# Optimization experiments

Measured on AMD Instinct MI355X. Metric: run time of the kernel, lower is better.

## Reference

```python
import jax, jax.numpy as jnp
import numpy as np

B, Y = 1024, 50000
MAX_TRIALS = 4096


def setup_inputs() -> dict:
    key = jax.random.key(0)
    k1, k2 = jax.random.split(key)
    input_ = jax.random.normal(k1, (B, Y), dtype=jnp.float32)
    pos = jax.random.randint(k2, (B,), 0, Y)
    target = jnp.zeros((B, Y), jnp.float32).at[jnp.arange(B), pos].set(1.0)
    return {"input_": input_, "target": target, "max_num_trials": MAX_TRIALS}


def reference(input_, target, max_num_trials):
    """WARP loss. The torch original sequentially samples negatives WITHOUT
    replacement per row until margin 1 + s_neg - s_pos >= 0 or max_num_trials
    is hit. Sampling without replacement == taking a uniform random
    permutation of the negative labels and scanning it; the first violating
    position t gives num_trials = t+1. This lets us fully vectorize the
    irregular loop while computing identical math (up to RNG stream)."""
    Bn, Yn = input_.shape
    rows = jnp.arange(Bn)
    pos = jnp.argmax(target, axis=1)                 # one positive per row (as J[i,1])
    pos_score = input_[rows, pos]                    # [B]

    # uniform random permutation of the Y-1 negatives per row:
    # random sort keys, force the positive label to sort last, drop it.
    u = jax.random.uniform(jax.random.key(42), (Bn, Yn))
    u = u.at[rows, pos].set(2.0)
    perm = jnp.argsort(u, axis=1)[:, : Yn - 1]       # [B, Y-1] negative label ids

    neg_scores = jnp.take_along_axis(input_, perm, axis=1)   # [B, Y-1]
    margins = 1.0 + neg_scores - pos_score[:, None]
    trial_ok = jnp.arange(Yn - 1)[None, :] < max_num_trials
    viol = (margins >= 0.0) & trial_ok
    found = jnp.any(viol, axis=1)
    first = jnp.argmax(viol, axis=1)                 # first violating trial index
    num_trials = (first + 1).astype(jnp.float32)
    # loss_weight = log(floor((Y-1)/num_trials)); 0 when no violator found
    L = jnp.where(found, jnp.log(jnp.floor((Yn - 1.0) / num_trials)), 0.0)
    neg_score = jnp.where(
        found, jnp.take_along_axis(neg_scores, first[:, None], axis=1)[:, 0], 0.0
    )
    loss = L * (1.0 - pos_score + neg_score)         # [B]
    return jnp.sum(loss, keepdims=True)              # shape (1,), as torch.sum(dim=0, keepdim=True)
```

## Files before the change

### kernel.cpp

```cpp
#include <hip/hip_runtime.h>
#include <stdint.h>

#define BN 1024
#define YN 50000
#define NTOT (BN * YN)
#define NGROUPS (NTOT / 4)
#define CAP 96
#define BITS_T (1u << 22)
#define HASH_BLOCKS 4096
#define STRIDE (HASH_BLOCKS * 256)

#define ROTL(x, r) __builtin_amdgcn_alignbit((x), (x), 32u - (r))
#define RND(b, a, r) { b += a; a = ROTL(a, r); a ^= b; }
#define RND4(r) { RND(b0,a0,r) RND(b1,a1,r) RND(b2,a2,r) RND(b3,a3,r) }
#define INJ4(db, da) { b0 += (db); b1 += (db); b2 += (db); b3 += (db); \
                       a0 += (da); a1 += (da); a2 += (da); a3 += (da); }

__device__ __forceinline__ uint32_t tf_bits(uint32_t ctr) {
    const uint32_t ks1 = 42u, ks2 = 0x1BD11BF0u;
    uint32_t x0 = 0u, x1 = ctr + ks1;
#define TFR(r) { x0 += x1; x1 = ROTL(x1, r); x1 ^= x0; }
    TFR(13) TFR(15) TFR(26) TFR(6)
    x0 += ks1; x1 += ks2 + 1u;
    TFR(17) TFR(29) TFR(16) TFR(24)
    x0 += ks2; x1 += 2u;
    TFR(13) TFR(15) TFR(26) TFR(6)
    x1 += ks1 + 3u;
    TFR(17) TFR(29) TFR(16) TFR(24)
    x0 += ks1; x1 += ks2 + 4u;
    TFR(13) TFR(15) TFR(26) TFR(6)
    x0 += ks2; x1 += 5u;
    return x0 ^ x1;
}

struct WS {
    uint32_t* cnt; int* pos; float* ps; float* row_loss; int* flag; uint32_t* cand;
};
static inline WS ws_layout(void* d_ws) {
    uint32_t* p = (uint32_t*)d_ws;
    WS w;
    w.cnt = p; w.pos = (int*)(p + BN); w.ps = (float*)(p + 2 * BN);
    w.row_loss = (float*)(p + 3 * BN); w.flag = (int*)(p + 4 * BN);
    w.cand = p + 5 * BN;
    return w;
}

__global__ __launch_bounds__(256, 4) void gen_kernel(
    const float* __restrict__ input, const float* __restrict__ target,
    uint32_t* __restrict__ cnt, uint32_t* __restrict__ cand,
    int* __restrict__ pos_out, float* __restrict__ ps_out)
{
    const int tid = threadIdx.x;
    if (blockIdx.x < BN) {
        const int row = blockIdx.x;
        const size_t base = (size_t)row * YN;
        __shared__ volatile int s_pos;
        if (tid == 0) s_pos = -1;
        __syncthreads();
        const float4* t4 = (const float4*)(target + base);
        for (int j4 = tid; j4 < YN / 4; j4 += 256) {
            if (s_pos >= 0) break;
            float4 v = t4[j4];
            int c0 = 4 * j4;
            if (v.x != 0.0f) s_pos = c0;
            if (v.y != 0.0f) s_pos = c0 + 1;
            if (v.z != 0.0f) s_pos = c0 + 2;
            if (v.w != 0.0f) s_pos = c0 + 3;
        }
        __syncthreads();
        if (tid == 0) {
            int p = s_pos;
            pos_out[row] = p;
            ps_out[row] = input[base + p];
        }
        return;
    }
    const uint32_t gid = (uint32_t)(blockIdx.x - BN) * 256u + (uint32_t)tid;
    const uint32_t ks1 = 42u, ks2 = 0x1BD11BF0u;
    for (uint32_t g = gid; g < NGROUPS; g += STRIDE) {
        const uint32_t c4 = g << 2;
        uint32_t a0 = c4 + 42u, a1 = c4 + 43u, a2 = c4 + 44u, a3 = c4 + 45u;
        uint32_t b0 = 0u, b1 = 0u, b2 = 0u, b3 = 0u;
        RND4(13) RND4(15) RND4(26) RND4(6)
        INJ4(ks1, ks2 + 1u)
        RND4(17) RND4(29) RND4(16) RND4(24)
        INJ4(ks2, 2u)
        RND4(13) RND4(15) RND4(26) RND4(6)
        INJ4(0u, ks1 + 3u)
        RND4(17) RND4(29) RND4(16) RND4(24)
        INJ4(ks1, ks2 + 4u)
        RND4(13) RND4(15) RND4(26) RND4(6)
        INJ4(ks2, 5u)
        const uint32_t o0 = b0 ^ a0, o1 = b1 ^ a1, o2 = b2 ^ a2, o3 = b3 ^ a3;
        const uint32_t m01 = o0 < o1 ? o0 : o1;
        const uint32_t m23 = o2 < o3 ? o2 : o3;
        const uint32_t m = m01 < m23 ? m01 : m23;
        if (__builtin_expect(m < BITS_T, 0)) {
            const uint32_t os[4] = {o0, o1, o2, o3};
#pragma unroll
            for (int k = 0; k < 4; ++k) {
                if (os[k] < BITS_T) {
                    const uint32_t idx = c4 + (uint32_t)k;
                    const uint32_t row = idx / 50000u;
                    const uint32_t col = idx - row * 50000u;
                    const uint32_t slot = atomicAdd(&cnt[row], 1u);
                    if (slot < CAP)
                        cand[row * CAP + slot] = ((os[k] >> 9) << 17) | col;
                }
            }
        }
    }
}

__global__ __launch_bounds__(256) void resolve_kernel(
    const float* __restrict__ input, const uint32_t* __restrict__ cnt,
    const uint32_t* __restrict__ cand, const int* __restrict__ pos_,
    const float* __restrict__ ps_, const int* __restrict__ mt_ptr,
    float* __restrict__ row_loss, int* __restrict__ flag)
{
    const int gtid = blockIdx.x * 256 + threadIdx.x;
    const int row = gtid >> 6;
    const int lane = gtid & 63;
    const uint32_t n = cnt[row];
    if (n > CAP) { if (lane == 0) flag[row] = 1; return; }
    const int pos = pos_[row];
    const float ps = ps_[row];
    const uint32_t* cl = cand + row * CAP;
    const float* rowp = input + (size_t)row * YN;

    uint32_t e0 = 0xFFFFFFFFu, e1 = 0xFFFFFFFFu;
    if ((uint32_t)lane < n) e0 = cl[lane];
    if ((uint32_t)(lane + 64) < n) e1 = cl[lane + 64];

    uint32_t mk = 0xFFFFFFFFu;
    {
        int col = (int)(e0 & 0x1FFFFu);
        if (e0 != 0xFFFFFFFFu && col != pos &&
            (1.0f + rowp[col]) - ps >= 0.0f) mk = e0;
        col = (int)(e1 & 0x1FFFFu);
        if (e1 != 0xFFFFFFFFu && col != pos &&
            (1.0f + rowp[col]) - ps >= 0.0f && e1 < mk) mk = e1;
    }
    for (int off = 32; off > 0; off >>= 1) {
        uint32_t o = (uint32_t)__shfl_xor((int)mk, off, 64);
        mk = (o < mk) ? o : mk;
    }
    if (mk == 0xFFFFFFFFu) {
        if (lane == 0) flag[row] = 1;
        return;
    }
    uint32_t c = 0;
    c += (e0 < mk && (int)(e0 & 0x1FFFFu) != pos) ? 1u : 0u;
    c += (e1 < mk && (int)(e1 & 0x1FFFFu) != pos) ? 1u : 0u;
    for (int off = 32; off > 0; off >>= 1) c += (uint32_t)__shfl_xor((int)c, off, 64);
    if (lane == 0) {
        flag[row] = 0;
        float loss = 0.0f;
        if (c < (uint32_t)mt_ptr[0]) {
            int cstar = (int)(mk & 0x1FFFFu);
            float ns = rowp[cstar];
            float nt = (float)(c + 1u);
            loss = logf(floorf(49999.0f / nt)) * ((1.0f - ps) + ns);
        }
        row_loss[row] = loss;
    }
}

__global__ __launch_bounds__(256) void fallback_kernel(
    const float* __restrict__ input, const int* __restrict__ flag,
    const int* __restrict__ pos_, const float* __restrict__ ps_,
    const int* __restrict__ mt_ptr, float* __restrict__ row_loss)
{
    const int row = blockIdx.x;
    if (!flag[row]) return;
    const int tid = threadIdx.x;
    const int pos = pos_[row];
    const float ps = ps_[row];
    const uint32_t base32 = (uint32_t)row * (uint32_t)YN;
    const float* rowp = input + (size_t)row * YN;

    __shared__ uint64_t smin[256];
    __shared__ uint32_t ssum[256];

    uint64_t mk = ~0ull;
    for (int col = tid; col < YN; col += 256) {
        uint32_t bits = tf_bits(base32 + (uint32_t)col);
        uint64_t key = ((uint64_t)(bits >> 9) << 17) | (uint32_t)col;
        float mrg = (1.0f + rowp[col]) - ps;
        if ((mrg >= 0.0f) && (col != pos) && (key < mk)) mk = key;
    }
    smin[tid] = mk;
    __syncthreads();
    for (int s = 128; s > 0; s >>= 1) {
        if (tid < s) { uint64_t o = smin[tid + s]; if (o < smin[tid]) smin[tid] = o; }
        __syncthreads();
    }
    const uint64_t kstar = smin[0];
    if (kstar == ~0ull) {
        if (tid == 0) row_loss[row] = 0.0f;
        return;
    }
    uint32_t c = 0;
    for (int col = tid; col < YN; col += 256) {
        uint32_t bits = tf_bits(base32 + (uint32_t)col);
        uint64_t key = ((uint64_t)(bits >> 9) << 17) | (uint32_t)col;
        c += ((key < kstar) && (col != pos)) ? 1u : 0u;
    }
    ssum[tid] = c;
    __syncthreads();
    for (int s = 128; s > 0; s >>= 1) {
        if (tid < s) ssum[tid] += ssum[tid + s];
        __syncthreads();
    }
    if (tid == 0) {
        uint32_t rank = ssum[0];
        float loss = 0.0f;
        if (rank < (uint32_t)mt_ptr[0]) {
            int cstar = (int)(kstar & 0x1FFFFull);
            float ns = rowp[cstar];
            float nt = (float)(rank + 1u);
            loss = logf(floorf(49999.0f / nt)) * ((1.0f - ps) + ns);
        }
        row_loss[row] = loss;
    }
}

__global__ __launch_bounds__(256) void reduce_kernel(
    const float* __restrict__ row_loss, float* __restrict__ out)
{
    __shared__ float s[256];
    int tid = threadIdx.x;
    float acc = 0.0f;
    for (int i = tid; i < BN; i += 256) acc += row_loss[i];
    s[tid] = acc;
    __syncthreads();
    for (int st = 128; st > 0; st >>= 1) {
        if (tid < st) s[tid] += s[tid + st];
        __syncthreads();
    }
    if (tid == 0) out[0] = s[0];
}

extern "C" void kernel_launch(void* const* d_in, const int* in_sizes, int n_in,
                              void* d_out, int out_size, void* d_ws, size_t ws_size,
                              hipStream_t stream) {
    const float* input  = (const float*)d_in[0];
    const float* target = (const float*)d_in[1];
    const int*   mt     = (const int*)d_in[2];
    float* out = (float*)d_out;
    WS w = ws_layout(d_ws);

    hipMemsetAsync(w.cnt, 0, BN * sizeof(uint32_t), stream);
    gen_kernel<<<BN + HASH_BLOCKS, 256, 0, stream>>>(
        input, target, w.cnt, w.cand, w.pos, w.ps);
    resolve_kernel<<<BN / 4, 256, 0, stream>>>(
        input, w.cnt, w.cand, w.pos, w.ps, mt, w.row_loss, w.flag);
    fallback_kernel<<<BN, 256, 0, stream>>>(
        input, w.flag, w.pos, w.ps, mt, w.row_loss);
    reduce_kernel<<<1, 256, 0, stream>>>(w.row_loss, out);
}
```

Baseline: 541.7 us.

## Hash eight counters per thread and fuse resolve with fallback kernel

The random-bits generator now computes eight Threefry counters per thread with fixed grid-strided iterations, replacing four per thread in a loop, to raise instruction-level parallelism and cut loop overhead. The launch-bounds occupancy hint is dropped. The resolve and fallback kernels are merged into one block-per-row kernel, which removes one launch and the flag array. The cost is higher register pressure in the hash loop and a full block per row during candidate resolution, where a single wavefront used to suffice.

Measured after the change: 536.5 us. Within noise of the previous version (-1.0%).

```diff
diff --git a/kernel.cpp b/kernel.cpp
--- a/kernel.cpp
+++ b/kernel.cpp
@@ -3,18 +3,20 @@
 
 #define BN 1024
 #define YN 50000
-#define NTOT (BN * YN)
-#define NGROUPS (NTOT / 4)
 #define CAP 96
 #define BITS_T (1u << 22)
-#define HASH_BLOCKS 4096
-#define STRIDE (HASH_BLOCKS * 256)
+#define SCANB BN
+#define HASHB 5000
+#define ITERS 5
 
 #define ROTL(x, r) __builtin_amdgcn_alignbit((x), (x), 32u - (r))
 #define RND(b, a, r) { b += a; a = ROTL(a, r); a ^= b; }
-#define RND4(r) { RND(b0,a0,r) RND(b1,a1,r) RND(b2,a2,r) RND(b3,a3,r) }
-#define INJ4(db, da) { b0 += (db); b1 += (db); b2 += (db); b3 += (db); \
-                       a0 += (da); a1 += (da); a2 += (da); a3 += (da); }
+#define R8(r) { RND(b0,a0,r) RND(b1,a1,r) RND(b2,a2,r) RND(b3,a3,r) \
+                RND(b4,a4,r) RND(b5,a5,r) RND(b6,a6,r) RND(b7,a7,r) }
+#define IB8(db) { b0 += (db); b1 += (db); b2 += (db); b3 += (db); \
+                  b4 += (db); b5 += (db); b6 += (db); b7 += (db); }
+#define IA8(da) { a0 += (da); a1 += (da); a2 += (da); a3 += (da); \
+                  a4 += (da); a5 += (da); a6 += (da); a7 += (da); }
 
 __device__ __forceinline__ uint32_t tf_bits(uint32_t ctr) {
     const uint32_t ks1 = 42u, ks2 = 0x1BD11BF0u;
@@ -33,25 +35,22 @@
     return x0 ^ x1;
 }
 
-struct WS {
-    uint32_t* cnt; int* pos; float* ps; float* row_loss; int* flag; uint32_t* cand;
-};
+struct WS { uint32_t* cnt; int* pos; float* ps; float* row_loss; uint32_t* cand; };
 static inline WS ws_layout(void* d_ws) {
     uint32_t* p = (uint32_t*)d_ws;
     WS w;
     w.cnt = p; w.pos = (int*)(p + BN); w.ps = (float*)(p + 2 * BN);
-    w.row_loss = (float*)(p + 3 * BN); w.flag = (int*)(p + 4 * BN);
-    w.cand = p + 5 * BN;
+    w.row_loss = (float*)(p + 3 * BN); w.cand = p + 4 * BN;
     return w;
 }
 
-__global__ __launch_bounds__(256, 4) void gen_kernel(
+__global__ __launch_bounds__(256) void gen_kernel(
     const float* __restrict__ input, const float* __restrict__ target,
     uint32_t* __restrict__ cnt, uint32_t* __restrict__ cand,
     int* __restrict__ pos_out, float* __restrict__ ps_out)
 {
     const int tid = threadIdx.x;
-    if (blockIdx.x < BN) {
+    if (blockIdx.x < SCANB) {
         const int row = blockIdx.x;
         const size_t base = (size_t)row * YN;
         __shared__ volatile int s_pos;
@@ -75,32 +74,37 @@
         }
         return;
     }
-    const uint32_t gid = (uint32_t)(blockIdx.x - BN) * 256u + (uint32_t)tid;
+    const uint32_t hb = (uint32_t)(blockIdx.x - SCANB);
     const uint32_t ks1 = 42u, ks2 = 0x1BD11BF0u;
-    for (uint32_t g = gid; g < NGROUPS; g += STRIDE) {
-        const uint32_t c4 = g << 2;
-        uint32_t a0 = c4 + 42u, a1 = c4 + 43u, a2 = c4 + 44u, a3 = c4 + 45u;
+#pragma unroll 1
+    for (uint32_t it = 0; it < ITERS; ++it) {
+        const uint32_t chunk = (it * HASHB + hb) * 256u + (uint32_t)tid;
+        const uint32_t c8 = chunk * 8u;
+        uint32_t a0 = c8 + 42u, a1 = c8 + 43u, a2 = c8 + 44u, a3 = c8 + 45u;
+        uint32_t a4 = c8 + 46u, a5 = c8 + 47u, a6 = c8 + 48u, a7 = c8 + 49u;
         uint32_t b0 = 0u, b1 = 0u, b2 = 0u, b3 = 0u;
-        RND4(13) RND4(15) RND4(26) RND4(6)
-        INJ4(ks1, ks2 + 1u)
-        RND4(17) RND4(29) RND4(16) RND4(24)
-        INJ4(ks2, 2u)
-        RND4(13) RND4(15) RND4(26) RND4(6)
-        INJ4(0u, ks1 + 3u)
-        RND4(17) RND4(29) RND4(16) RND4(24)
-        INJ4(ks1, ks2 + 4u)
-        RND4(13) RND4(15) RND4(26) RND4(6)
-        INJ4(ks2, 5u)
+        uint32_t b4 = 0u, b5 = 0u, b6 = 0u, b7 = 0u;
+        R8(13) R8(15) R8(26) R8(6)
+        IB8(ks1) IA8(ks2 + 1u)
+        R8(17) R8(29) R8(16) R8(24)
+        IB8(ks2) IA8(2u)
+        R8(13) R8(15) R8(26) R8(6)
+        IA8(ks1 + 3u)
+        R8(17) R8(29) R8(16) R8(24)
+        IB8(ks1) IA8(ks2 + 4u)
+        R8(13) R8(15) R8(26) R8(6)
+        IB8(ks2) IA8(5u)
         const uint32_t o0 = b0 ^ a0, o1 = b1 ^ a1, o2 = b2 ^ a2, o3 = b3 ^ a3;
-        const uint32_t m01 = o0 < o1 ? o0 : o1;
-        const uint32_t m23 = o2 < o3 ? o2 : o3;
-        const uint32_t m = m01 < m23 ? m01 : m23;
-        if (__builtin_expect(m < BITS_T, 0)) {
-            const uint32_t os[4] = {o0, o1, o2, o3};
+        const uint32_t o4 = b4 ^ a4, o5 = b5 ^ a5, o6 = b6 ^ a6, o7 = b7 ^ a7;
+        uint32_t m01 = o0 < o1 ? o0 : o1,  m23 = o2 < o3 ? o2 : o3;
+        uint32_t m45 = o4 < o5 ? o4 : o5,  m67 = o6 < o7 ? o6 : o7;
+        uint32_t mA = m01 < m23 ? m01 : m23, mB = m45 < m67 ? m45 : m67;
+        if (__builtin_expect((mA < mB ? mA : mB) < BITS_T, 0)) {
+            const uint32_t os[8] = {o0, o1, o2, o3, o4, o5, o6, o7};
 #pragma unroll
-            for (int k = 0; k < 4; ++k) {
+            for (int k = 0; k < 8; ++k) {
                 if (os[k] < BITS_T) {
-                    const uint32_t idx = c4 + (uint32_t)k;
+                    const uint32_t idx = c8 + (uint32_t)k;
                     const uint32_t row = idx / 50000u;
                     const uint32_t col = idx - row * 50000u;
                     const uint32_t slot = atomicAdd(&cnt[row], 1u);
@@ -112,76 +116,64 @@
     }
 }
 
-__global__ __launch_bounds__(256) void resolve_kernel(
+__global__ __launch_bounds__(256) void resolve_fb_kernel(
     const float* __restrict__ input, const uint32_t* __restrict__ cnt,
     const uint32_t* __restrict__ cand, const int* __restrict__ pos_,
     const float* __restrict__ ps_, const int* __restrict__ mt_ptr,
-    float* __restrict__ row_loss, int* __restrict__ flag)
+    float* __restrict__ row_loss)
 {
-    const int gtid = blockIdx.x * 256 + threadIdx.x;
-    const int row = gtid >> 6;
-    const int lane = gtid & 63;
+    const int row = blockIdx.x;
+    const int tid = threadIdx.x;
     const uint32_t n = cnt[row];
-    if (n > CAP) { if (lane == 0) flag[row] = 1; return; }
     const int pos = pos_[row];
     const float ps = ps_[row];
-    const uint32_t* cl = cand + row * CAP;
     const float* rowp = input + (size_t)row * YN;
-
-    uint32_t e0 = 0xFFFFFFFFu, e1 = 0xFFFFFFFFu;
-    if ((uint32_t)lane < n) e0 = cl[lane];
-    if ((uint32_t)(lane + 64) < n) e1 = cl[lane + 64];
-
-    uint32_t mk = 0xFFFFFFFFu;
-    {
-        int col = (int)(e0 & 0x1FFFFu);
-        if (e0 != 0xFFFFFFFFu && col != pos &&
-            (1.0f + rowp[col]) - ps >= 0.0f) mk = e0;
-        col = (int)(e1 & 0x1FFFFu);
-        if (e1 != 0xFFFFFFFFu && col != pos &&
-            (1.0f + rowp[col]) - ps >= 0.0f && e1 < mk) mk = e1;
-    }
-    for (int off = 32; off > 0; off >>= 1) {
-        uint32_t o = (uint32_t)__shfl_xor((int)mk, off, 64);
-        mk = (o < mk) ? o : mk;
-    }
-    if (mk == 0xFFFFFFFFu) {
-        if (lane == 0) flag[row] = 1;
-        return;
-    }
-    uint32_t c = 0;
-    c += (e0 < mk && (int)(e0 & 0x1FFFFu) != pos) ? 1u : 0u;
-    c += (e1 < mk && (int)(e1 & 0x1FFFFu) != pos) ? 1u : 0u;
-    for (int off = 32; off > 0; off >>= 1) c += (uint32_t)__shfl_xor((int)c, off, 64);
-    if (lane == 0) {
-        flag[row] = 0;
-        float loss = 0.0f;
-        if (c < (uint32_t)mt_ptr[0]) {
-            int cstar = (int)(mk & 0x1FFFFu);
-            float ns = rowp[cstar];
-            float nt = (float)(c + 1u);
-            loss = logf(floorf(49999.0f / nt)) * ((1.0f - ps) + ns);
-        }
-        row_loss[row] = loss;
-    }
-}
-
-__global__ __launch_bounds__(256) void fallback_kernel(
-    const float* __restrict__ input, const int* __restrict__ flag,
-    const int* __restrict__ pos_, const float* __restrict__ ps_,
-    const int* __restrict__ mt_ptr, float* __restrict__ row_loss)
-{
-    const int row = blockIdx.x;
-    if (!flag[row]) return;
-    const int tid = threadIdx.x;
-    const int pos = pos_[row];
-    const float ps = ps_[row];
+    const uint32_t maxt = (uint32_t)mt_ptr[0];
+
+    __shared__ uint32_t s32[256];
+    bool need_fallback = (n > CAP);
+
+    if (!need_fallback) {
+        const uint32_t* cl = cand + row * CAP;
+        uint32_t e = 0xFFFFFFFFu;
+        int ecol = -1;
+        if ((uint32_t)tid < n) { e = cl[tid]; ecol = (int)(e & 0x1FFFFu); }
+        uint32_t mk = 0xFFFFFFFFu;
+        if (ecol >= 0 && ecol != pos && (1.0f + rowp[ecol]) - ps >= 0.0f) mk = e;
+        s32[tid] = mk;
+        __syncthreads();
+        for (int s = 128; s > 0; s >>= 1) {
+            if (tid < s) { uint32_t o = s32[tid + s]; if (o < s32[tid]) s32[tid] = o; }
+            __syncthreads();
+        }
+        mk = s32[0];
+        __syncthreads();
+        if (mk != 0xFFFFFFFFu) {
+            uint32_t c = (e < mk && ecol != pos) ? 1u : 0u;
+            s32[tid] = c;
+            __syncthreads();
+            for (int s = 128; s > 0; s >>= 1) {
+                if (tid < s) s32[tid] += s32[tid + s];
+                __syncthreads();
+            }
+            if (tid == 0) {
+                uint32_t rank = s32[0];
+                float loss = 0.0f;
+                if (rank < maxt) {
+                    int cstar = (int)(mk & 0x1FFFFu);
+                    float ns = rowp[cstar];
+                    float nt = (float)(rank + 1u);
+                    loss = logf(floorf(49999.0f / nt)) * ((1.0f - ps) + ns);
+                }
+                row_loss[row] = loss;
+            }
+            return;
+        }
+        need_fallback = true;
+    }
+
+    __shared__ uint64_t s64[256];
     const uint32_t base32 = (uint32_t)row * (uint32_t)YN;
-    const float* rowp = input + (size_t)row * YN;
-
-    __shared__ uint64_t smin[256];
-    __shared__ uint32_t ssum[256];
-
     uint64_t mk = ~0ull;
     for (int col = tid; col < YN; col += 256) {
         uint32_t bits = tf_bits(base32 + (uint32_t)col);
@@ -189,13 +181,13 @@
         float mrg = (1.0f + rowp[col]) - ps;
         if ((mrg >= 0.0f) && (col != pos) && (key < mk)) mk = key;
     }
-    smin[tid] = mk;
+    s64[tid] = mk;
     __syncthreads();
     for (int s = 128; s > 0; s >>= 1) {
-        if (tid < s) { uint64_t o = smin[tid + s]; if (o < smin[tid]) smin[tid] = o; }
-        __syncthreads();
-    }
-    const uint64_t kstar = smin[0];
+        if (tid < s) { uint64_t o = s64[tid + s]; if (o < s64[tid]) s64[tid] = o; }
+        __syncthreads();
+    }
+    const uint64_t kstar = s64[0];
     if (kstar == ~0ull) {
         if (tid == 0) row_loss[row] = 0.0f;
         return;
@@ -206,16 +198,16 @@
         uint64_t key = ((uint64_t)(bits >> 9) << 17) | (uint32_t)col;
         c += ((key < kstar) && (col != pos)) ? 1u : 0u;
     }
-    ssum[tid] = c;
+    s32[tid] = c;
     __syncthreads();
     for (int s = 128; s > 0; s >>= 1) {
-        if (tid < s) ssum[tid] += ssum[tid + s];
+        if (tid < s) s32[tid] += s32[tid + s];
         __syncthreads();
     }
     if (tid == 0) {
-        uint32_t rank = ssum[0];
+        uint32_t rank = s32[0];
         float loss = 0.0f;
-        if (rank < (uint32_t)mt_ptr[0]) {
+        if (rank < maxt) {
             int cstar = (int)(kstar & 0x1FFFFull);
             float ns = rowp[cstar];
             float nt = (float)(rank + 1u);
@@ -251,11 +243,9 @@
     WS w = ws_layout(d_ws);
 
     hipMemsetAsync(w.cnt, 0, BN * sizeof(uint32_t), stream);
-    gen_kernel<<<BN + HASH_BLOCKS, 256, 0, stream>>>(
+    gen_kernel<<<SCANB + HASHB, 256, 0, stream>>>(
         input, target, w.cnt, w.cand, w.pos, w.ps);
-    resolve_kernel<<<BN / 4, 256, 0, stream>>>(
-        input, w.cnt, w.cand, w.pos, w.ps, mt, w.row_loss, w.flag);
-    fallback_kernel<<<BN, 256, 0, stream>>>(
-        input, w.flag, w.pos, w.ps, mt, w.row_loss);
+    resolve_fb_kernel<<<BN, 256, 0, stream>>>(
+        input, w.cnt, w.cand, w.pos, w.ps, mt, w.row_loss);
     reduce_kernel<<<1, 256, 0, stream>>>(w.row_loss, out);
 }
```
